# Kernel tuning notes

Measured on AMD Instinct MI355X. Metric: run time of the kernel, lower is better.

The kernel has to match this reference:

```python
import jax, jax.numpy as jnp
from jax import lax
import numpy as np

B, T, F, H, C = 32, 1000, 161, 512, 62

def setup_inputs() -> dict:
    key = jax.random.key(0)
    ks = jax.random.split(key, 12)
    s = lambda *sh: 1.0 / np.sqrt(sh[0])
    inp = {
        'x': jax.random.normal(ks[0], (B, T, F), jnp.float32),
        'seq_lens': jax.random.randint(ks[1], (B,), T // 2, T + 1, jnp.int32),
        'w1': jax.random.normal(ks[2], (F, H), jnp.float32) * s(F),
        'b1': jnp.zeros((H,), jnp.float32),
        'w2': jax.random.normal(ks[3], (H, H), jnp.float32) * s(H),
        'b2': jnp.zeros((H,), jnp.float32),
        'wg_f': jax.random.normal(ks[4], (2 * H, 2 * H), jnp.float32) * s(2 * H),
        'bg_f': jnp.ones((2 * H,), jnp.float32),  # TF GRU gate bias init = 1.0
        'wc_f': jax.random.normal(ks[5], (2 * H, H), jnp.float32) * s(2 * H),
        'bc_f': jnp.zeros((H,), jnp.float32),
        'wg_b': jax.random.normal(ks[6], (2 * H, 2 * H), jnp.float32) * s(2 * H),
        'bg_b': jnp.ones((2 * H,), jnp.float32),
        'wc_b': jax.random.normal(ks[7], (2 * H, H), jnp.float32) * s(2 * H),
        'bc_b': jnp.zeros((H,), jnp.float32),
        'wf': jax.random.normal(ks[8], (2 * H, C), jnp.float32) * s(2 * H),
        'bf': jnp.zeros((C,), jnp.float32),
    }
    return inp


def _reverse_sequence(x, lens):
    # mimic tf.reverse_sequence along time axis 1
    t = jnp.arange(x.shape[1])  # [T]
    idx = jnp.where(t[None, :] < lens[:, None], lens[:, None] - 1 - t[None, :], t[None, :])  # [B,T]
    return jnp.take_along_axis(x, idx[:, :, None], axis=1)


def _run_gru(x, lens, wg, bg, wc, bc):
    # x: [B,T,H] -> outputs [B,T,H]; zero output and frozen state past lens (dynamic_rnn semantics)
    xT = jnp.swapaxes(x, 0, 1)  # [T,B,H]
    h0 = jnp.zeros((x.shape[0], bc.shape[0]), x.dtype)

    def step(h, inp):
        xt, t = inp
        ru = jax.nn.sigmoid(jnp.concatenate([xt, h], axis=-1) @ wg + bg)
        r, u = jnp.split(ru, 2, axis=-1)
        c = jnp.tanh(jnp.concatenate([xt, r * h], axis=-1) @ wc + bc)
        hn = u * h + (1.0 - u) * c
        mask = (t < lens)[:, None]
        h_new = jnp.where(mask, hn, h)
        out = jnp.where(mask, hn, jnp.zeros_like(hn))
        return h_new, out

    _, outs = lax.scan(step, h0, (xT, jnp.arange(x.shape[1])))
    return jnp.swapaxes(outs, 0, 1)


def reference(x, seq_lens, w1, b1, w2, b2, wg_f, bg_f, wc_f, bc_f, wg_b, bg_b, wc_b, bc_b, wf, bf):
    h = jax.nn.relu(x @ w1 + b1)
    h = jax.nn.relu(h @ w2 + b2)  # [B,T,H]
    out_f = _run_gru(h, seq_lens, wg_f, bg_f, wc_f, bc_f)
    h_rev = _reverse_sequence(h, seq_lens)
    out_b = _reverse_sequence(_run_gru(h_rev, seq_lens, wg_b, bg_b, wc_b, bc_b), seq_lens)
    scores = jnp.concatenate([out_f, out_b], axis=2)  # [B,T,2H]
    logits = scores @ wf + bf  # [B,T,C]
    return logits
```

## Files before the change

### kernel.cpp

```cpp
#include <hip/hip_runtime.h>
#include <hip/hip_bf16.h>
#include <cstdint>

#define B_  32
#define T_  1000
#define F_  161
#define H_  512
#define C_  62
#define BT_ 32000
#define TC  200
#define NCH 5
#define MCH (B_ * TC)
#define ESC_TRIES (1 << 14)

typedef __bf16 bf16x8 __attribute__((ext_vector_type(8)));
typedef float  f32x4  __attribute__((ext_vector_type(4)));
typedef unsigned short us8 __attribute__((ext_vector_type(8)));

__device__ __forceinline__ float b2f(unsigned short s) {
    union { unsigned int i; float f; } v; v.i = (unsigned int)s << 16; return v.f;
}
__device__ __forceinline__ unsigned short f2b(float f) {
    unsigned int u = __float_as_uint(f);
    unsigned int r = u + 0x7fffu + ((u >> 16) & 1u);
    return (unsigned short)(r >> 16);
}


__global__ __launch_bounds__(256) void cvt_x_pad(const float* __restrict__ x,
                                                 unsigned short* __restrict__ xb) {
    int idx = blockIdx.x * 256 + threadIdx.x;
    if (idx >= BT_ * 192) return;
    int r = idx / 192, k = idx - r * 192;
    float v = (k < F_) ? x[(size_t)r * F_ + k] : 0.f;
    xb[idx] = f2b(v);
}

__global__ __launch_bounds__(256) void transpose_cvt(const float* __restrict__ src,
                                                     unsigned short* __restrict__ dst,
                                                     int K, int N, int k0, int KP, int NP) {
    int idx = blockIdx.x * 256 + threadIdx.x;
    if (idx >= NP * KP) return;
    int n = idx / KP, k = idx - n * KP;
    float v = (k < K && n < N) ? src[(size_t)(k0 + k) * N + n] : 0.f;
    dst[idx] = f2b(v);
}

__global__ __launch_bounds__(256) void biascat(const float* __restrict__ bg_f,
                                               const float* __restrict__ bc_f,
                                               const float* __restrict__ bg_b,
                                               const float* __restrict__ bc_b,
                                               float* __restrict__ bcat) {
    int idx = blockIdx.x * 256 + threadIdx.x;
    if (idx >= 2 * 1536) return;
    int d = idx / 1536, c = idx - d * 1536;
    const float* bg = d ? bg_b : bg_f;
    const float* bc = d ? bc_b : bc_f;
    bcat[idx] = (c < 1024) ? bg[c] : bc[c - 1024];
}


#define BM 128
#define BN 64
#define BK 64

template<bool RELU, int OMODE, bool AMAP>
__global__ __launch_bounds__(256) void gemm_bf16(const unsigned short* __restrict__ A,
                                                 const unsigned short* __restrict__ BT,
                                                 const float* __restrict__ bias,
                                                 void* __restrict__ Out,
                                                 int K, int Nreal, int t0) {
    __shared__ __align__(16) unsigned short As[BM * BK];
    __shared__ __align__(16) unsigned short Bs[BN * BK];
    const int tid  = threadIdx.x;
    const int lane = tid & 63;
    const int w    = tid >> 6;
    const int wm   = w & 1, wn = w >> 1;
    const int l15  = lane & 15, l4 = lane >> 4;
    const int m0   = blockIdx.x * BM;
    const int n0   = blockIdx.y * BN;

    const int ar = tid >> 1, ac = (tid & 1) * 32;
    const int br = tid >> 2, bc = (tid & 3) * 16;

    size_t arow;
    {
        int r = m0 + ar;
        if (AMAP) { int rb = r / TC; int rt = r - rb * TC; arow = (size_t)rb * T_ + t0 + rt; }
        else      arow = (size_t)r;
    }

    f32x4 acc[4][2] = {};

    for (int kt = 0; kt < K; kt += BK) {
        if (kt) __syncthreads();
        {
            const unsigned short* ga = A + arow * K + kt + ac;
            us8* la = (us8*)(As + ar * BK + ac);
            #pragma unroll
            for (int j = 0; j < 4; ++j) la[j] = *(const us8*)(ga + 8 * j);
            const unsigned short* gb = BT + (size_t)(n0 + br) * K + kt + bc;
            us8* lb = (us8*)(Bs + br * BK + bc);
            #pragma unroll
            for (int j = 0; j < 2; ++j) lb[j] = *(const us8*)(gb + 8 * j);
        }
        __syncthreads();
        #pragma unroll
        for (int kk = 0; kk < BK; kk += 32) {
            bf16x8 af[4], bfr[2];
            #pragma unroll
            for (int m = 0; m < 4; ++m)
                af[m] = *(const bf16x8*)(As + (wm * 64 + m * 16 + l15) * BK + kk + l4 * 8);
            #pragma unroll
            for (int n = 0; n < 2; ++n)
                bfr[n] = *(const bf16x8*)(Bs + (wn * 32 + n * 16 + l15) * BK + kk + l4 * 8);
            #pragma unroll
            for (int m = 0; m < 4; ++m)
                #pragma unroll
                for (int n = 0; n < 2; ++n)
                    acc[m][n] = __builtin_amdgcn_mfma_f32_16x16x32_bf16(af[m], bfr[n], acc[m][n], 0, 0, 0);
        }
    }

    const int rbase = m0 + wm * 64;
    const int cb    = n0 + wn * 32;
    #pragma unroll
    for (int m = 0; m < 4; ++m) {
        #pragma unroll
        for (int n = 0; n < 2; ++n) {
            int gc = cb + n * 16 + l15;
            if (gc < Nreal) {
                float bv = bias ? bias[gc] : 0.f;
                int gr0 = rbase + m * 16 + l4 * 4;
                #pragma unroll
                for (int r = 0; r < 4; ++r) {
                    float v = acc[m][n][r] + bv;
                    if (RELU) v = fmaxf(v, 0.f);
                    int gr = gr0 + r;
                    if (OMODE == 0) {
                        ((unsigned short*)Out)[(size_t)gr * Nreal + gc] = f2b(v);
                    } else {
                        int rb = gr / TC; int rt = gr - rb * TC;
                        size_t orow = (size_t)rb * T_ + t0 + rt;
                        ((float*)Out)[orow * Nreal + gc] += v;
                    }
                }
            }
        }
    }
}


__device__ __forceinline__ void wait_flag(const unsigned int* f, unsigned int tgt) {
    int tries = 0;
    while (__hip_atomic_load(f, __ATOMIC_RELAXED, __HIP_MEMORY_SCOPE_AGENT) < tgt) {
        if (++tries >= ESC_TRIES) break;
        __builtin_amdgcn_s_sleep(1);
    }
    asm volatile("" ::: "memory");
}

__device__ __forceinline__ void stage_peer(unsigned short* STG, const unsigned int* src,
                                           int q, int lane) {
    const unsigned long long* s64 = (const unsigned long long*)src;
    int row = lane >> 1, half = lane & 1;
    const unsigned long long* a = s64 + row * 128 + 8 * q + 4 * half;
    unsigned long long d0 = __hip_atomic_load(a + 0, __ATOMIC_RELAXED, __HIP_MEMORY_SCOPE_AGENT);
    unsigned long long d1 = __hip_atomic_load(a + 1, __ATOMIC_RELAXED, __HIP_MEMORY_SCOPE_AGENT);
    unsigned long long d2 = __hip_atomic_load(a + 2, __ATOMIC_RELAXED, __HIP_MEMORY_SCOPE_AGENT);
    unsigned long long d3 = __hip_atomic_load(a + 3, __ATOMIC_RELAXED, __HIP_MEMORY_SCOPE_AGENT);
    int bb  = 64 * q + 32 * half;
    int swz = (row & 7) << 4;
    char* rp = (char*)STG + row * 1024;
    *(unsigned long long*)(rp + ((bb +  0) ^ swz)) = d0;
    *(unsigned long long*)(rp + ((bb +  8) ^ swz)) = d1;
    *(unsigned long long*)(rp + ((bb + 16) ^ swz)) = d2;
    *(unsigned long long*)(rp + ((bb + 24) ^ swz)) = d3;
}

__global__ __launch_bounds__(512) void gru_persist(const unsigned short* __restrict__ wh_f,
                                                   const unsigned short* __restrict__ wh_b,
                                                   const unsigned short* __restrict__ Xf,
                                                   const unsigned short* __restrict__ Xb,
                                                   const int* __restrict__ seq_lens,
                                                   float* __restrict__ hf32_glob,
                                                   unsigned int* __restrict__ hb_g,
                                                   unsigned int* __restrict__ rh_g,
                                                   unsigned int* __restrict__ fH_g,
                                                   unsigned int* __restrict__ fR_g,
                                                   int* __restrict__ claim,
                                                   unsigned short* __restrict__ of,
                                                   unsigned short* __restrict__ ob,
                                                   int t0f, int t0b, int base, int init) {
    __shared__ __align__(16) unsigned short WG[64 * 512];
    __shared__ __align__(16) unsigned short WC[32 * 512];
    __shared__ __align__(16) unsigned short STG[32 * 512];
    __shared__ __align__(16) unsigned short XGs[32 * 64];
    __shared__ __align__(16) unsigned short XCs[32 * 32];
    __shared__ float USH[32][33];
    __shared__ float HOWN[32][32];
    __shared__ int Ls[32];
    __shared__ int role_sh;

    const int tid = threadIdx.x;

    if (tid == 0) {
        unsigned int xcd;
        asm volatile("s_getreg_b32 %0, hwreg(HW_REG_XCC_ID)" : "=s"(xcd));
        xcd &= 7u;
        int r = -1;
        if (xcd < 2u) {
            int s = atomicAdd(&claim[xcd], 1);
            if (s < 16) r = (int)(xcd * 16u) + s;
        }
        role_sh = r;
    }
    __syncthreads();
    const int role = role_sh;
    if (role < 0) return;
    const int dir = role >> 4;
    const int g   = role & 15;

    const int lane = tid & 63;
    const int w   = tid >> 6;
    const int l15 = lane & 15, l4 = lane >> 4;

    const unsigned short* wh = dir ? wh_b : wh_f;
    const unsigned short* X  = dir ? Xb : Xf;
    unsigned short* out      = dir ? ob : of;
    const int t0 = dir ? t0b : t0f;
    float*        hf32 = hf32_glob + (size_t)dir * 32 * 512;
    unsigned int* hb0 = hb_g + (size_t)dir * 2 * 8192;
    unsigned int* rh0 = rh_g + (size_t)dir * 2 * 8192;
    unsigned int* fH  = fH_g + dir * 256;
    unsigned int* fR  = fR_g + dir * 256;
    unsigned int* myfH = fH + g * 16;
    unsigned int* myfR = fR + g * 16;

    for (int j = tid; j < 4096; j += 512) {
        int col = j >> 6, ck = j & 63;
        int srcc = (col < 32) ? (32 * g + col) : (512 + 32 * g + (col - 32));
        int dstb = col * 1024 + ((ck * 16) ^ ((col & 7) << 4));
        *(us8*)((char*)WG + dstb) = *(const us8*)(wh + (size_t)srcc * 512 + ck * 8);
    }
    for (int j = tid; j < 2048; j += 512) {
        int col = j >> 6, ck = j & 63;
        int dstb = col * 1024 + ((ck * 16) ^ ((col & 7) << 4));
        *(us8*)((char*)WC + dstb) = *(const us8*)(wh + (size_t)(1024 + 32 * g + col) * 512 + ck * 8);
    }
    if (tid < 32) {
        int L = seq_lens[tid];
        Ls[tid] = L < 0 ? 0 : (L > T_ ? T_ : L);
    }
    for (int j = tid; j < 1024; j += 512) {
        int row = j >> 5, lc = j & 31;
        HOWN[row][lc] = init ? 0.f : hf32[row * 512 + 32 * g + lc];
    }
    {
        int tt0 = dir ? (TC - 1) : 0;
        if (tid < 256) {
            int b = tid >> 3, part = tid & 7;
            int srcc = (part < 4) ? (32 * g + part * 8) : (512 + 32 * g + (part - 4) * 8);
            *(us8*)(XGs + b * 64 + part * 8) =
                *(const us8*)(X + ((size_t)b * TC + tt0) * 1536 + srcc);
        }
    }

    const int mt = w & 1, nt = w >> 1;
    const int mt2 = w & 1, nt2 = (w >> 1) & 1;

    for (int i = 0; i < TC; ++i) {
        const int tt = dir ? (TC - 1 - i) : i;
        const int t  = t0 + tt;
        const unsigned int s = (unsigned)(base + i);

        if (init && i == 0) {
            for (int j = tid; j < 4096; j += 512)
                *(unsigned long long*)((char*)STG + j * 8) = 0ull;
        } else {
            const unsigned int* hbs = hb0 + ((s - 1) & 1) * 8192;
            #pragma unroll
            for (int k = 0; k < 2; ++k) {
                int q = 2 * w + k;
                wait_flag(fH + q * 16, s);
                stage_peer(STG, hbs, q, lane);
            }
        }
        if (tid < 128) {
            int b = tid >> 2, part = tid & 3;
            *(us8*)(XCs + b * 32 + part * 8) =
                *(const us8*)(X + ((size_t)b * TC + tt) * 1536 + 1024 + 32 * g + part * 8);
        }
        __syncthreads();

        f32x4 acc = {};
        {
            const int arow = mt * 16 + l15;
            const int bcol = nt * 16 + l15;
            const int sa = (arow & 7) << 4, sb2 = (bcol & 7) << 4;
            const char* pa = (const char*)STG + arow * 1024;
            const char* pb = (const char*)WG + bcol * 1024;
            #pragma unroll
            for (int kk = 0; kk < 16; ++kk) {
                int kb = kk * 64 + l4 * 16;
                bf16x8 a  = *(const bf16x8*)(pa + (kb ^ sa));
                bf16x8 bf = *(const bf16x8*)(pb + (kb ^ sb2));
                acc = __builtin_amdgcn_mfma_f32_16x16x32_bf16(a, bf, acc, 0, 0, 0);
            }
        }
        {
            unsigned int* rhs = rh0 + (s & 1) * 8192;
            const int colL = nt * 16 + l15;
            #pragma unroll
            for (int r = 0; r < 4; ++r) {
                int row = mt * 16 + l4 * 4 + r;
                float sv = acc[r] + b2f(XGs[row * 64 + colL]);
                float sg = 1.f / (1.f + __expf(-sv));
                if (colL < 32) {
                    int c = 32 * g + colL;
                    unsigned short ho = *(const unsigned short*)((const char*)STG + row * 1024 +
                                            ((c * 2) ^ ((row & 7) << 4)));
                    unsigned int pr = f2b(sg * b2f(ho));
                    unsigned int po = (unsigned int)__shfl_xor((int)pr, 1);
                    if (!(lane & 1))
                        __hip_atomic_store(rhs + row * 256 + 16 * g + (colL >> 1),
                                           pr | (po << 16),
                                           __ATOMIC_RELAXED, __HIP_MEMORY_SCOPE_AGENT);
                } else {
                    USH[row][colL - 32] = sg;
                }
            }
        }
        __syncthreads();
        if (tid == 0)
            __hip_atomic_store(myfR, s + 1, __ATOMIC_RELAXED, __HIP_MEMORY_SCOPE_AGENT);

        {
            const unsigned int* rhs = rh0 + (s & 1) * 8192;
            #pragma unroll
            for (int k = 0; k < 2; ++k) {
                int q = 2 * w + k;
                wait_flag(fR + q * 16, s + 1);
                stage_peer(STG, rhs, q, lane);
            }
        }
        __syncthreads();

        if (w < 4) {
            f32x4 acc2 = {};
            const int arow = mt2 * 16 + l15;
            const int bcol = nt2 * 16 + l15;
            const int sa = (arow & 7) << 4, sb2 = (bcol & 7) << 4;
            const char* pa = (const char*)STG + arow * 1024;
            const char* pb = (const char*)WC + bcol * 1024;
            #pragma unroll
            for (int kk = 0; kk < 16; ++kk) {
                int kb = kk * 64 + l4 * 16;
                bf16x8 a  = *(const bf16x8*)(pa + (kb ^ sa));
                bf16x8 bf = *(const bf16x8*)(pb + (kb ^ sb2));
                acc2 = __builtin_amdgcn_mfma_f32_16x16x32_bf16(a, bf, acc2, 0, 0, 0);
            }
            unsigned int* hbs = hb0 + (s & 1) * 8192;
            const int colL2 = nt2 * 16 + l15;
            const int col_c = 32 * g + colL2;
            #pragma unroll
            for (int r = 0; r < 4; ++r) {
                int row = mt2 * 16 + l4 * 4 + r;
                float sv = acc2[r] + b2f(XCs[row * 32 + colL2]);
                float cv = tanhf(sv);
                float uu = USH[row][colL2];
                float ho = HOWN[row][colL2];
                bool act = (t < Ls[row]);
                float hn = act ? (uu * ho + (1.f - uu) * cv) : ho;
                unsigned short hnb = f2b(hn);
                out[((size_t)row * TC + tt) * 512 + col_c] = act ? hnb : (unsigned short)0;
                unsigned int ph = hnb;
                unsigned int po = (unsigned int)__shfl_xor((int)ph, 1);
                if (!(lane & 1))
                    __hip_atomic_store(hbs + row * 256 + 16 * g + (colL2 >> 1),
                                       ph | (po << 16),
                                       __ATOMIC_RELAXED, __HIP_MEMORY_SCOPE_AGENT);
                HOWN[row][colL2] = hn;
            }
        } else if (i + 1 < TC) {
            int ttn = dir ? (tt - 1) : (tt + 1);
            int jd = tid - 256;
            int b = jd >> 3, part = jd & 7;
            int srcc = (part < 4) ? (32 * g + part * 8) : (512 + 32 * g + (part - 4) * 8);
            *(us8*)(XGs + b * 64 + part * 8) =
                *(const us8*)(X + ((size_t)b * TC + ttn) * 1536 + srcc);
        }
        __syncthreads();
        if (tid == 0)
            __hip_atomic_store(myfH, s + 1, __ATOMIC_RELAXED, __HIP_MEMORY_SCOPE_AGENT);
    }

    for (int j = tid; j < 1024; j += 512) {
        int row = j >> 5, lc = j & 31;
        hf32[row * 512 + 32 * g + lc] = HOWN[row][lc];
    }
}


extern "C" void kernel_launch(void* const* d_in, const int* in_sizes, int n_in,
                              void* d_out, int out_size, void* d_ws, size_t ws_size,
                              hipStream_t stream) {
    (void)in_sizes; (void)n_in; (void)out_size; (void)ws_size;
    const float* x    = (const float*)d_in[0];
    const int*   seq  = (const int*)  d_in[1];
    const float* w1   = (const float*)d_in[2];
    const float* b1   = (const float*)d_in[3];
    const float* w2   = (const float*)d_in[4];
    const float* b2   = (const float*)d_in[5];
    const float* wg_f = (const float*)d_in[6];
    const float* bg_f = (const float*)d_in[7];
    const float* wc_f = (const float*)d_in[8];
    const float* bc_f = (const float*)d_in[9];
    const float* wg_b = (const float*)d_in[10];
    const float* bg_b = (const float*)d_in[11];
    const float* wc_b = (const float*)d_in[12];
    const float* bc_b = (const float*)d_in[13];
    const float* wf   = (const float*)d_in[14];
    const float* bfv  = (const float*)d_in[15];

    char* p = (char*)d_ws;
    auto alloc = [&](size_t bytes) { char* q = p; p += (bytes + 255) & ~(size_t)255; return q; };

    unsigned short* w1T     = (unsigned short*)alloc(512 * 192 * 2);
    unsigned short* w2T     = (unsigned short*)alloc(512 * 512 * 2);
    unsigned short* wx_f    = (unsigned short*)alloc((size_t)1536 * 512 * 2);
    unsigned short* wx_b    = (unsigned short*)alloc((size_t)1536 * 512 * 2);
    unsigned short* wh_f    = (unsigned short*)alloc((size_t)1536 * 512 * 2);
    unsigned short* wh_b    = (unsigned short*)alloc((size_t)1536 * 512 * 2);
    unsigned short* wfT_top = (unsigned short*)alloc(64 * 512 * 2);
    unsigned short* wfT_bot = (unsigned short*)alloc(64 * 512 * 2);
    float*          bcat    = (float*)         alloc(2 * 1536 * 4);

    unsigned short* hB = (unsigned short*)alloc((size_t)BT_ * 512 * 2);

    char* U = alloc((size_t)MCH * 1536 * 2 * 2 + (size_t)MCH * 512 * 2 * 2);
    unsigned short* xb = (unsigned short*)U;
    unsigned short* h1 = (unsigned short*)(U + (size_t)BT_ * 192 * 2);
    unsigned short* Xf = (unsigned short*)U;
    unsigned short* Xb = (unsigned short*)(U + (size_t)MCH * 1536 * 2);
    unsigned short* of = (unsigned short*)(U + (size_t)MCH * 1536 * 2 * 2);
    unsigned short* ob = (unsigned short*)(U + (size_t)MCH * 1536 * 2 * 2 + (size_t)MCH * 512 * 2);

    unsigned int*   fH_gl    = (unsigned int*)alloc(2 * 256 * 4);
    unsigned int*   fR_gl    = (unsigned int*)alloc(2 * 256 * 4);
    int*            claim    = (int*)         alloc(256);
    float*          hf32_gl  = (float*)       alloc((size_t)2 * 32 * 512 * 4);
    unsigned int*   hb_gl    = (unsigned int*)alloc((size_t)2 * 2 * 8192 * 4);
    unsigned int*   rh_gl    = (unsigned int*)alloc((size_t)2 * 2 * 8192 * 4);

    hipMemsetAsync(d_out, 0, (size_t)BT_ * C_ * 4, stream);
    hipMemsetAsync(fH_gl, 0, 2 * 256 * 4 + 2 * 256 * 4 + 256, stream);

    transpose_cvt<<<(512 * 192) / 256, 256, 0, stream>>>(w1, w1T, 161, 512, 0, 192, 512);
    transpose_cvt<<<(512 * 512) / 256, 256, 0, stream>>>(w2, w2T, 512, 512, 0, 512, 512);
    transpose_cvt<<<(1024 * 512) / 256, 256, 0, stream>>>(wg_f, wx_f, 512, 1024, 0, 512, 1024);
    transpose_cvt<<<(512 * 512) / 256, 256, 0, stream>>>(wc_f, wx_f + (size_t)1024 * 512, 512, 512, 0, 512, 512);
    transpose_cvt<<<(1024 * 512) / 256, 256, 0, stream>>>(wg_b, wx_b, 512, 1024, 0, 512, 1024);
    transpose_cvt<<<(512 * 512) / 256, 256, 0, stream>>>(wc_b, wx_b + (size_t)1024 * 512, 512, 512, 0, 512, 512);
    transpose_cvt<<<(1024 * 512) / 256, 256, 0, stream>>>(wg_f, wh_f, 512, 1024, 512, 512, 1024);
    transpose_cvt<<<(512 * 512) / 256, 256, 0, stream>>>(wc_f, wh_f + (size_t)1024 * 512, 512, 512, 512, 512, 512);
    transpose_cvt<<<(1024 * 512) / 256, 256, 0, stream>>>(wg_b, wh_b, 512, 1024, 512, 512, 1024);
    transpose_cvt<<<(512 * 512) / 256, 256, 0, stream>>>(wc_b, wh_b + (size_t)1024 * 512, 512, 512, 512, 512, 512);
    transpose_cvt<<<(64 * 512) / 256, 256, 0, stream>>>(wf, wfT_top, 512, 62, 0, 512, 64);
    transpose_cvt<<<(64 * 512) / 256, 256, 0, stream>>>(wf, wfT_bot, 512, 62, 512, 512, 64);
    biascat<<<(2 * 1536 + 255) / 256, 256, 0, stream>>>(bg_f, bc_f, bg_b, bc_b, bcat);

    cvt_x_pad<<<(BT_ * 192 + 255) / 256, 256, 0, stream>>>(x, xb);
    gemm_bf16<true, 0, false><<<dim3(BT_ / BM, 512 / BN), 256, 0, stream>>>(xb, w1T, b1, h1, 192, 512, 0);
    gemm_bf16<true, 0, false><<<dim3(BT_ / BM, 512 / BN), 256, 0, stream>>>(h1, w2T, b2, hB, 512, 512, 0);

    for (int c = 0; c < NCH; ++c) {
        const int t0f = c * TC;
        const int t0b = (NCH - 1 - c) * TC;
        gemm_bf16<false, 0, true><<<dim3(MCH / BM, 1536 / BN), 256, 0, stream>>>(hB, wx_f, bcat,        Xf, 512, 1536, t0f);
        gemm_bf16<false, 0, true><<<dim3(MCH / BM, 1536 / BN), 256, 0, stream>>>(hB, wx_b, bcat + 1536, Xb, 512, 1536, t0b);
        gru_persist<<<256, 512, 0, stream>>>(wh_f, wh_b, Xf, Xb, seq, hf32_gl,
                                             hb_gl, rh_gl, fH_gl, fR_gl, claim + 2 * c,
                                             of, ob, t0f, t0b, c * TC, c == 0 ? 1 : 0);
        gemm_bf16<false, 1, false><<<dim3(MCH / BM, 1), 256, 0, stream>>>(of, wfT_top, bfv,     d_out, 512, C_, t0f);
        gemm_bf16<false, 1, false><<<dim3(MCH / BM, 1), 256, 0, stream>>>(ob, wfT_bot, nullptr, d_out, 512, C_, t0b);
    }
}
```

Baseline: 7.963 ms.

## Replace per-block ready flags with step tags embedded in exchanged data words

Each 32-bit packed pair of hidden or reset values is now stored in a 64-bit word whose upper half carries the step tag. Consumers poll the data words directly until every tag matches, instead of waiting on a separate per-block flag and then loading the data. This removes the flag store, the barrier-ordered flag round trip and the second load pass on the per-step critical path. In exchange the exchange buffers double in size, so each poll moves twice the bytes, and polling now issues eight loads per retry.

Result: slower. 11.60 ms (+45.7%).

```diff
diff --git a/kernel.cpp b/kernel.cpp
--- a/kernel.cpp
+++ b/kernel.cpp
@@ -151,31 +151,36 @@
 }
 
 
-__device__ __forceinline__ void wait_flag(const unsigned int* f, unsigned int tgt) {
+__device__ __forceinline__ void poll_stage(unsigned short* STG,
+                                           const unsigned long long* mb,
+                                           unsigned int tag, int q, int lane) {
+    int row = lane >> 1, half = lane & 1;
+    const unsigned long long* a = mb + row * 256 + 16 * q + 8 * half;
+    unsigned long long v[8];
+    unsigned int pend = 0xffu;
     int tries = 0;
-    while (__hip_atomic_load(f, __ATOMIC_RELAXED, __HIP_MEMORY_SCOPE_AGENT) < tgt) {
+    while (pend) {
+        #pragma unroll
+        for (int k = 0; k < 8; ++k)
+            if (pend & (1u << k))
+                v[k] = __hip_atomic_load(a + k, __ATOMIC_RELAXED, __HIP_MEMORY_SCOPE_AGENT);
+        #pragma unroll
+        for (int k = 0; k < 8; ++k)
+            if ((pend & (1u << k)) && (unsigned int)(v[k] >> 32) == tag)
+                pend &= ~(1u << k);
+        if (!pend) break;
         if (++tries >= ESC_TRIES) break;
         __builtin_amdgcn_s_sleep(1);
     }
     asm volatile("" ::: "memory");
-}
-
-__device__ __forceinline__ void stage_peer(unsigned short* STG, const unsigned int* src,
-                                           int q, int lane) {
-    const unsigned long long* s64 = (const unsigned long long*)src;
-    int row = lane >> 1, half = lane & 1;
-    const unsigned long long* a = s64 + row * 128 + 8 * q + 4 * half;
-    unsigned long long d0 = __hip_atomic_load(a + 0, __ATOMIC_RELAXED, __HIP_MEMORY_SCOPE_AGENT);
-    unsigned long long d1 = __hip_atomic_load(a + 1, __ATOMIC_RELAXED, __HIP_MEMORY_SCOPE_AGENT);
-    unsigned long long d2 = __hip_atomic_load(a + 2, __ATOMIC_RELAXED, __HIP_MEMORY_SCOPE_AGENT);
-    unsigned long long d3 = __hip_atomic_load(a + 3, __ATOMIC_RELAXED, __HIP_MEMORY_SCOPE_AGENT);
-    int bb  = 64 * q + 32 * half;
+    int base = 64 * q + 32 * half;
     int swz = (row & 7) << 4;
     char* rp = (char*)STG + row * 1024;
-    *(unsigned long long*)(rp + ((bb +  0) ^ swz)) = d0;
-    *(unsigned long long*)(rp + ((bb +  8) ^ swz)) = d1;
-    *(unsigned long long*)(rp + ((bb + 16) ^ swz)) = d2;
-    *(unsigned long long*)(rp + ((bb + 24) ^ swz)) = d3;
+    #pragma unroll
+    for (int k = 0; k < 4; ++k) {
+        unsigned long long d = (v[2 * k] & 0xffffffffull) | (v[2 * k + 1] << 32);
+        *(unsigned long long*)(rp + ((base + 8 * k) ^ swz)) = d;
+    }
 }
 
 __global__ __launch_bounds__(512) void gru_persist(const unsigned short* __restrict__ wh_f,
@@ -184,10 +189,8 @@
                                                    const unsigned short* __restrict__ Xb,
                                                    const int* __restrict__ seq_lens,
                                                    float* __restrict__ hf32_glob,
-                                                   unsigned int* __restrict__ hb_g,
-                                                   unsigned int* __restrict__ rh_g,
-                                                   unsigned int* __restrict__ fH_g,
-                                                   unsigned int* __restrict__ fR_g,
+                                                   unsigned long long* __restrict__ hb_g,
+                                                   unsigned long long* __restrict__ rh_g,
                                                    int* __restrict__ claim,
                                                    unsigned short* __restrict__ of,
                                                    unsigned short* __restrict__ ob,
@@ -229,13 +232,9 @@
     const unsigned short* X  = dir ? Xb : Xf;
     unsigned short* out      = dir ? ob : of;
     const int t0 = dir ? t0b : t0f;
-    float*        hf32 = hf32_glob + (size_t)dir * 32 * 512;
-    unsigned int* hb0 = hb_g + (size_t)dir * 2 * 8192;
-    unsigned int* rh0 = rh_g + (size_t)dir * 2 * 8192;
-    unsigned int* fH  = fH_g + dir * 256;
-    unsigned int* fR  = fR_g + dir * 256;
-    unsigned int* myfH = fH + g * 16;
-    unsigned int* myfR = fR + g * 16;
+    float*              hf32 = hf32_glob + (size_t)dir * 32 * 512;
+    unsigned long long* hb0 = hb_g + (size_t)dir * 2 * 8192;
+    unsigned long long* rh0 = rh_g + (size_t)dir * 2 * 8192;
 
     for (int j = tid; j < 4096; j += 512) {
         int col = j >> 6, ck = j & 63;
@@ -278,13 +277,9 @@
             for (int j = tid; j < 4096; j += 512)
                 *(unsigned long long*)((char*)STG + j * 8) = 0ull;
         } else {
-            const unsigned int* hbs = hb0 + ((s - 1) & 1) * 8192;
-            #pragma unroll
-            for (int k = 0; k < 2; ++k) {
-                int q = 2 * w + k;
-                wait_flag(fH + q * 16, s);
-                stage_peer(STG, hbs, q, lane);
-            }
+            const unsigned long long* hbs = hb0 + ((s - 1) & 1) * 8192;
+            poll_stage(STG, hbs, s, 2 * w, lane);
+            poll_stage(STG, hbs, s, 2 * w + 1, lane);
         }
         if (tid < 128) {
             int b = tid >> 2, part = tid & 3;
@@ -309,7 +304,8 @@
             }
         }
         {
-            unsigned int* rhs = rh0 + (s & 1) * 8192;
+            unsigned long long* rhs = rh0 + (s & 1) * 8192;
+            const unsigned long long tagw = ((unsigned long long)(s + 1)) << 32;
             const int colL = nt * 16 + l15;
             #pragma unroll
             for (int r = 0; r < 4; ++r) {
@@ -324,7 +320,7 @@
                     unsigned int po = (unsigned int)__shfl_xor((int)pr, 1);
                     if (!(lane & 1))
                         __hip_atomic_store(rhs + row * 256 + 16 * g + (colL >> 1),
-                                           pr | (po << 16),
+                                           tagw | pr | (po << 16),
                                            __ATOMIC_RELAXED, __HIP_MEMORY_SCOPE_AGENT);
                 } else {
                     USH[row][colL - 32] = sg;
@@ -332,17 +328,11 @@
             }
         }
         __syncthreads();
-        if (tid == 0)
-            __hip_atomic_store(myfR, s + 1, __ATOMIC_RELAXED, __HIP_MEMORY_SCOPE_AGENT);
 
         {
-            const unsigned int* rhs = rh0 + (s & 1) * 8192;
-            #pragma unroll
-            for (int k = 0; k < 2; ++k) {
-                int q = 2 * w + k;
-                wait_flag(fR + q * 16, s + 1);
-                stage_peer(STG, rhs, q, lane);
-            }
+            const unsigned long long* rhs = rh0 + (s & 1) * 8192;
+            poll_stage(STG, rhs, s + 1, 2 * w, lane);
+            poll_stage(STG, rhs, s + 1, 2 * w + 1, lane);
         }
         __syncthreads();
 
@@ -360,7 +350,8 @@
                 bf16x8 bf = *(const bf16x8*)(pb + (kb ^ sb2));
                 acc2 = __builtin_amdgcn_mfma_f32_16x16x32_bf16(a, bf, acc2, 0, 0, 0);
             }
-            unsigned int* hbs = hb0 + (s & 1) * 8192;
+            unsigned long long* hbs = hb0 + (s & 1) * 8192;
+            const unsigned long long tagw = ((unsigned long long)(s + 1)) << 32;
             const int colL2 = nt2 * 16 + l15;
             const int col_c = 32 * g + colL2;
             #pragma unroll
@@ -378,7 +369,7 @@
                 unsigned int po = (unsigned int)__shfl_xor((int)ph, 1);
                 if (!(lane & 1))
                     __hip_atomic_store(hbs + row * 256 + 16 * g + (colL2 >> 1),
-                                       ph | (po << 16),
+                                       tagw | ph | (po << 16),
                                        __ATOMIC_RELAXED, __HIP_MEMORY_SCOPE_AGENT);
                 HOWN[row][colL2] = hn;
             }
@@ -391,8 +382,6 @@
                 *(const us8*)(X + ((size_t)b * TC + ttn) * 1536 + srcc);
         }
         __syncthreads();
-        if (tid == 0)
-            __hip_atomic_store(myfH, s + 1, __ATOMIC_RELAXED, __HIP_MEMORY_SCOPE_AGENT);
     }
 
     for (int j = tid; j < 1024; j += 512) {
@@ -446,15 +435,13 @@
     unsigned short* of = (unsigned short*)(U + (size_t)MCH * 1536 * 2 * 2);
     unsigned short* ob = (unsigned short*)(U + (size_t)MCH * 1536 * 2 * 2 + (size_t)MCH * 512 * 2);
 
-    unsigned int*   fH_gl    = (unsigned int*)alloc(2 * 256 * 4);
-    unsigned int*   fR_gl    = (unsigned int*)alloc(2 * 256 * 4);
-    int*            claim    = (int*)         alloc(256);
-    float*          hf32_gl  = (float*)       alloc((size_t)2 * 32 * 512 * 4);
-    unsigned int*   hb_gl    = (unsigned int*)alloc((size_t)2 * 2 * 8192 * 4);
-    unsigned int*   rh_gl    = (unsigned int*)alloc((size_t)2 * 2 * 8192 * 4);
+    int*                claim   = (int*)               alloc(256);
+    float*              hf32_gl = (float*)             alloc((size_t)2 * 32 * 512 * 4);
+    unsigned long long* hb_gl   = (unsigned long long*)alloc((size_t)2 * 2 * 8192 * 8);
+    unsigned long long* rh_gl   = (unsigned long long*)alloc((size_t)2 * 2 * 8192 * 8);
 
     hipMemsetAsync(d_out, 0, (size_t)BT_ * C_ * 4, stream);
-    hipMemsetAsync(fH_gl, 0, 2 * 256 * 4 + 2 * 256 * 4 + 256, stream);
+    hipMemsetAsync(claim, 0, 256, stream);
 
     transpose_cvt<<<(512 * 192) / 256, 256, 0, stream>>>(w1, w1T, 161, 512, 0, 192, 512);
     transpose_cvt<<<(512 * 512) / 256, 256, 0, stream>>>(w2, w2T, 512, 512, 0, 512, 512);
@@ -480,7 +467,7 @@
         gemm_bf16<false, 0, true><<<dim3(MCH / BM, 1536 / BN), 256, 0, stream>>>(hB, wx_f, bcat,        Xf, 512, 1536, t0f);
         gemm_bf16<false, 0, true><<<dim3(MCH / BM, 1536 / BN), 256, 0, stream>>>(hB, wx_b, bcat + 1536, Xb, 512, 1536, t0b);
         gru_persist<<<256, 512, 0, stream>>>(wh_f, wh_b, Xf, Xb, seq, hf32_gl,
-                                             hb_gl, rh_gl, fH_gl, fR_gl, claim + 2 * c,
+                                             hb_gl, rh_gl, claim + 2 * c,
                                              of, ob, t0f, t0b, c * TC, c == 0 ? 1 : 0);
         gemm_bf16<false, 1, false><<<dim3(MCH / BM, 1), 256, 0, stream>>>(of, wfT_top, bfv,     d_out, 512, C_, t0f);
         gemm_bf16<false, 1, false><<<dim3(MCH / BM, 1), 256, 0, stream>>>(ob, wfT_bot, nullptr, d_out, 512, C_, t0b);
```

## Load peer GRU state directly into MFMA fragments with per-wave flags

Applied to the files above, without the earlier changes.

Removes the LDS staging buffer for the peer hidden and reset-gated states. Each wave now reads its MFMA A-fragments straight from global memory after a single wave-wide poll over all 64 per-wave flags. Flags become per-wave: each wave drains its stores with s_waitcnt and publishes its own flag, so the block-wide barrier before signaling and one __syncthreads per step go away. The owned hidden state moves from LDS into registers. The cost is more fine-grained global loads in the MFMA loop and 4x more flag traffic, with the risk of weaker ordering guarantees under relaxed atomics.

New measurement: 14.04 ms. 76.3% more time.

```diff
diff --git a/kernel.cpp b/kernel.cpp
--- a/kernel.cpp
+++ b/kernel.cpp
@@ -151,31 +151,25 @@
 }
 
 
-__device__ __forceinline__ void wait_flag(const unsigned int* f, unsigned int tgt) {
+__device__ __forceinline__ void poll64(const unsigned int* f, unsigned int tgt, int lane) {
+    const unsigned int* fp = f + ((lane >> 2) << 4) + (lane & 3);
     int tries = 0;
-    while (__hip_atomic_load(f, __ATOMIC_RELAXED, __HIP_MEMORY_SCOPE_AGENT) < tgt) {
+    for (;;) {
+        unsigned int v = __hip_atomic_load(fp, __ATOMIC_RELAXED, __HIP_MEMORY_SCOPE_AGENT);
+        if (__all(v >= tgt)) break;
         if (++tries >= ESC_TRIES) break;
         __builtin_amdgcn_s_sleep(1);
     }
     asm volatile("" ::: "memory");
 }
 
-__device__ __forceinline__ void stage_peer(unsigned short* STG, const unsigned int* src,
-                                           int q, int lane) {
-    const unsigned long long* s64 = (const unsigned long long*)src;
-    int row = lane >> 1, half = lane & 1;
-    const unsigned long long* a = s64 + row * 128 + 8 * q + 4 * half;
-    unsigned long long d0 = __hip_atomic_load(a + 0, __ATOMIC_RELAXED, __HIP_MEMORY_SCOPE_AGENT);
+__device__ __forceinline__ bf16x8 frag_ld(const unsigned long long* mb, int row, int q, int l4) {
+    const unsigned long long* a = mb + row * 128 + 8 * q + 2 * l4;
+    unsigned long long d0 = __hip_atomic_load(a,     __ATOMIC_RELAXED, __HIP_MEMORY_SCOPE_AGENT);
     unsigned long long d1 = __hip_atomic_load(a + 1, __ATOMIC_RELAXED, __HIP_MEMORY_SCOPE_AGENT);
-    unsigned long long d2 = __hip_atomic_load(a + 2, __ATOMIC_RELAXED, __HIP_MEMORY_SCOPE_AGENT);
-    unsigned long long d3 = __hip_atomic_load(a + 3, __ATOMIC_RELAXED, __HIP_MEMORY_SCOPE_AGENT);
-    int bb  = 64 * q + 32 * half;
-    int swz = (row & 7) << 4;
-    char* rp = (char*)STG + row * 1024;
-    *(unsigned long long*)(rp + ((bb +  0) ^ swz)) = d0;
-    *(unsigned long long*)(rp + ((bb +  8) ^ swz)) = d1;
-    *(unsigned long long*)(rp + ((bb + 16) ^ swz)) = d2;
-    *(unsigned long long*)(rp + ((bb + 24) ^ swz)) = d3;
+    union { unsigned long long u[2]; bf16x8 v; } c;
+    c.u[0] = d0; c.u[1] = d1;
+    return c.v;
 }
 
 __global__ __launch_bounds__(512) void gru_persist(const unsigned short* __restrict__ wh_f,
@@ -194,11 +188,9 @@
                                                    int t0f, int t0b, int base, int init) {
     __shared__ __align__(16) unsigned short WG[64 * 512];
     __shared__ __align__(16) unsigned short WC[32 * 512];
-    __shared__ __align__(16) unsigned short STG[32 * 512];
     __shared__ __align__(16) unsigned short XGs[32 * 64];
     __shared__ __align__(16) unsigned short XCs[32 * 32];
     __shared__ float USH[32][33];
-    __shared__ float HOWN[32][32];
     __shared__ int Ls[32];
     __shared__ int role_sh;
 
@@ -234,8 +226,6 @@
     unsigned int* rh0 = rh_g + (size_t)dir * 2 * 8192;
     unsigned int* fH  = fH_g + dir * 256;
     unsigned int* fR  = fR_g + dir * 256;
-    unsigned int* myfH = fH + g * 16;
-    unsigned int* myfR = fR + g * 16;
 
     for (int j = tid; j < 4096; j += 512) {
         int col = j >> 6, ck = j & 63;
@@ -251,10 +241,6 @@
     if (tid < 32) {
         int L = seq_lens[tid];
         Ls[tid] = L < 0 ? 0 : (L > T_ ? T_ : L);
-    }
-    for (int j = tid; j < 1024; j += 512) {
-        int row = j >> 5, lc = j & 31;
-        HOWN[row][lc] = init ? 0.f : hf32[row * 512 + 32 * g + lc];
     }
     {
         int tt0 = dir ? (TC - 1) : 0;
@@ -269,96 +255,90 @@
     const int mt = w & 1, nt = w >> 1;
     const int mt2 = w & 1, nt2 = (w >> 1) & 1;
 
+    float hreg[4];
+    if (w < 4) {
+        #pragma unroll
+        for (int r = 0; r < 4; ++r) {
+            int row = mt2 * 16 + l4 * 4 + r;
+            hreg[r] = init ? 0.f : hf32[row * 512 + 32 * g + nt2 * 16 + l15];
+        }
+    }
+    __syncthreads();
+
     for (int i = 0; i < TC; ++i) {
         const int tt = dir ? (TC - 1 - i) : i;
         const int t  = t0 + tt;
         const unsigned int s = (unsigned)(base + i);
 
-        if (init && i == 0) {
-            for (int j = tid; j < 4096; j += 512)
-                *(unsigned long long*)((char*)STG + j * 8) = 0ull;
-        } else {
-            const unsigned int* hbs = hb0 + ((s - 1) & 1) * 8192;
-            #pragma unroll
-            for (int k = 0; k < 2; ++k) {
-                int q = 2 * w + k;
-                wait_flag(fH + q * 16, s);
-                stage_peer(STG, hbs, q, lane);
-            }
-        }
         if (tid < 128) {
             int b = tid >> 2, part = tid & 3;
             *(us8*)(XCs + b * 32 + part * 8) =
                 *(const us8*)(X + ((size_t)b * TC + tt) * 1536 + 1024 + 32 * g + part * 8);
         }
-        __syncthreads();
 
         f32x4 acc = {};
-        {
+        if (!(init && i == 0)) {
+            poll64(fH, s, lane);
+            const unsigned long long* hbs =
+                (const unsigned long long*)(hb0 + ((s - 1) & 1) * 8192);
             const int arow = mt * 16 + l15;
             const int bcol = nt * 16 + l15;
-            const int sa = (arow & 7) << 4, sb2 = (bcol & 7) << 4;
-            const char* pa = (const char*)STG + arow * 1024;
+            const int sb2 = (bcol & 7) << 4;
             const char* pb = (const char*)WG + bcol * 1024;
             #pragma unroll
-            for (int kk = 0; kk < 16; ++kk) {
-                int kb = kk * 64 + l4 * 16;
-                bf16x8 a  = *(const bf16x8*)(pa + (kb ^ sa));
-                bf16x8 bf = *(const bf16x8*)(pb + (kb ^ sb2));
-                acc = __builtin_amdgcn_mfma_f32_16x16x32_bf16(a, bf, acc, 0, 0, 0);
+            for (int q = 0; q < 16; ++q) {
+                bf16x8 afr = frag_ld(hbs, arow, q, l4);
+                bf16x8 bfr = *(const bf16x8*)(pb + ((q * 64 + l4 * 16) ^ sb2));
+                acc = __builtin_amdgcn_mfma_f32_16x16x32_bf16(afr, bfr, acc, 0, 0, 0);
             }
         }
+
         {
-            unsigned int* rhs = rh0 + (s & 1) * 8192;
             const int colL = nt * 16 + l15;
-            #pragma unroll
-            for (int r = 0; r < 4; ++r) {
-                int row = mt * 16 + l4 * 4 + r;
-                float sv = acc[r] + b2f(XGs[row * 64 + colL]);
-                float sg = 1.f / (1.f + __expf(-sv));
-                if (colL < 32) {
-                    int c = 32 * g + colL;
-                    unsigned short ho = *(const unsigned short*)((const char*)STG + row * 1024 +
-                                            ((c * 2) ^ ((row & 7) << 4)));
-                    unsigned int pr = f2b(sg * b2f(ho));
+            if (w < 4) {
+                unsigned int* rhs = rh0 + (s & 1) * 8192;
+                #pragma unroll
+                for (int r = 0; r < 4; ++r) {
+                    int row = mt * 16 + l4 * 4 + r;
+                    float sv = acc[r] + b2f(XGs[row * 64 + colL]);
+                    float sg = 1.f / (1.f + __expf(-sv));
+                    float ho = b2f(f2b(hreg[r]));
+                    unsigned int pr = f2b(sg * ho);
                     unsigned int po = (unsigned int)__shfl_xor((int)pr, 1);
                     if (!(lane & 1))
                         __hip_atomic_store(rhs + row * 256 + 16 * g + (colL >> 1),
                                            pr | (po << 16),
                                            __ATOMIC_RELAXED, __HIP_MEMORY_SCOPE_AGENT);
-                } else {
-                    USH[row][colL - 32] = sg;
+                }
+                asm volatile("s_waitcnt vmcnt(0)" ::: "memory");
+                if (lane == 0)
+                    __hip_atomic_store(fR + g * 16 + w, s + 1,
+                                       __ATOMIC_RELAXED, __HIP_MEMORY_SCOPE_AGENT);
+            } else {
+                #pragma unroll
+                for (int r = 0; r < 4; ++r) {
+                    int row = mt * 16 + l4 * 4 + r;
+                    float sv = acc[r] + b2f(XGs[row * 64 + colL]);
+                    USH[row][colL - 32] = 1.f / (1.f + __expf(-sv));
                 }
             }
         }
         __syncthreads();
-        if (tid == 0)
-            __hip_atomic_store(myfR, s + 1, __ATOMIC_RELAXED, __HIP_MEMORY_SCOPE_AGENT);
-
-        {
-            const unsigned int* rhs = rh0 + (s & 1) * 8192;
-            #pragma unroll
-            for (int k = 0; k < 2; ++k) {
-                int q = 2 * w + k;
-                wait_flag(fR + q * 16, s + 1);
-                stage_peer(STG, rhs, q, lane);
-            }
-        }
-        __syncthreads();
 
         if (w < 4) {
+            poll64(fR, s + 1, lane);
+            const unsigned long long* rhs =
+                (const unsigned long long*)(rh0 + (s & 1) * 8192);
             f32x4 acc2 = {};
             const int arow = mt2 * 16 + l15;
             const int bcol = nt2 * 16 + l15;
-            const int sa = (arow & 7) << 4, sb2 = (bcol & 7) << 4;
-            const char* pa = (const char*)STG + arow * 1024;
+            const int sb2 = (bcol & 7) << 4;
             const char* pb = (const char*)WC + bcol * 1024;
             #pragma unroll
-            for (int kk = 0; kk < 16; ++kk) {
-                int kb = kk * 64 + l4 * 16;
-                bf16x8 a  = *(const bf16x8*)(pa + (kb ^ sa));
-                bf16x8 bf = *(const bf16x8*)(pb + (kb ^ sb2));
-                acc2 = __builtin_amdgcn_mfma_f32_16x16x32_bf16(a, bf, acc2, 0, 0, 0);
+            for (int q = 0; q < 16; ++q) {
+                bf16x8 afr = frag_ld(rhs, arow, q, l4);
+                bf16x8 bfr = *(const bf16x8*)(pb + ((q * 64 + l4 * 16) ^ sb2));
+                acc2 = __builtin_amdgcn_mfma_f32_16x16x32_bf16(afr, bfr, acc2, 0, 0, 0);
             }
             unsigned int* hbs = hb0 + (s & 1) * 8192;
             const int colL2 = nt2 * 16 + l15;
@@ -369,7 +349,7 @@
                 float sv = acc2[r] + b2f(XCs[row * 32 + colL2]);
                 float cv = tanhf(sv);
                 float uu = USH[row][colL2];
-                float ho = HOWN[row][colL2];
+                float ho = hreg[r];
                 bool act = (t < Ls[row]);
                 float hn = act ? (uu * ho + (1.f - uu) * cv) : ho;
                 unsigned short hnb = f2b(hn);
@@ -380,8 +360,12 @@
                     __hip_atomic_store(hbs + row * 256 + 16 * g + (colL2 >> 1),
                                        ph | (po << 16),
                                        __ATOMIC_RELAXED, __HIP_MEMORY_SCOPE_AGENT);
-                HOWN[row][colL2] = hn;
+                hreg[r] = hn;
             }
+            asm volatile("s_waitcnt vmcnt(0)" ::: "memory");
+            if (lane == 0)
+                __hip_atomic_store(fH + g * 16 + w, s + 1,
+                                   __ATOMIC_RELAXED, __HIP_MEMORY_SCOPE_AGENT);
         } else if (i + 1 < TC) {
             int ttn = dir ? (tt - 1) : (tt + 1);
             int jd = tid - 256;
@@ -391,13 +375,14 @@
                 *(const us8*)(X + ((size_t)b * TC + ttn) * 1536 + srcc);
         }
         __syncthreads();
-        if (tid == 0)
-            __hip_atomic_store(myfH, s + 1, __ATOMIC_RELAXED, __HIP_MEMORY_SCOPE_AGENT);
-    }
-
-    for (int j = tid; j < 1024; j += 512) {
-        int row = j >> 5, lc = j & 31;
-        hf32[row * 512 + 32 * g + lc] = HOWN[row][lc];
+    }
+
+    if (w < 4) {
+        #pragma unroll
+        for (int r = 0; r < 4; ++r) {
+            int row = mt2 * 16 + l4 * 4 + r;
+            hf32[row * 512 + 32 * g + nt2 * 16 + l15] = hreg[r];
+        }
     }
 }
 
```

## Use per-wave flag publishing and wave-wide polling in persistent GRU recurrence

Applied to the files above, without the earlier changes.

Each of the four writer waves now publishes its own completion flag right after its stores drain (s_waitcnt vmcnt(0)), rather than one thread publishing a block-wide flag after a __syncthreads. Consumers poll all eight sub-flags of their two peer groups in parallel with one wave vote. The hidden state moves from the HOWN shared array into per-lane registers, and r*h is computed from those registers instead of being read back from staged shared memory. The intent is to cut a barrier and serial flag polls from the per-timestep cross-block handoff, at the cost of more flag traffic and reliance on relaxed-ordering memory semantics.

Result: slower. 8.613 ms (+8.2%).

```diff
diff --git a/kernel.cpp b/kernel.cpp
--- a/kernel.cpp
+++ b/kernel.cpp
@@ -151,9 +151,14 @@
 }
 
 
-__device__ __forceinline__ void wait_flag(const unsigned int* f, unsigned int tgt) {
+__device__ __forceinline__ void poll_sub(const unsigned int* f, unsigned int tgt,
+                                         int w, int lane) {
+    const unsigned int* fp = f + (2 * w + (lane >> 2)) * 16 + (lane & 3);
     int tries = 0;
-    while (__hip_atomic_load(f, __ATOMIC_RELAXED, __HIP_MEMORY_SCOPE_AGENT) < tgt) {
+    for (;;) {
+        unsigned int v = (lane < 8)
+            ? __hip_atomic_load(fp, __ATOMIC_RELAXED, __HIP_MEMORY_SCOPE_AGENT) : tgt;
+        if (__all(v >= tgt)) break;
         if (++tries >= ESC_TRIES) break;
         __builtin_amdgcn_s_sleep(1);
     }
@@ -198,7 +203,6 @@
     __shared__ __align__(16) unsigned short XGs[32 * 64];
     __shared__ __align__(16) unsigned short XCs[32 * 32];
     __shared__ float USH[32][33];
-    __shared__ float HOWN[32][32];
     __shared__ int Ls[32];
     __shared__ int role_sh;
 
@@ -234,8 +238,6 @@
     unsigned int* rh0 = rh_g + (size_t)dir * 2 * 8192;
     unsigned int* fH  = fH_g + dir * 256;
     unsigned int* fR  = fR_g + dir * 256;
-    unsigned int* myfH = fH + g * 16;
-    unsigned int* myfR = fR + g * 16;
 
     for (int j = tid; j < 4096; j += 512) {
         int col = j >> 6, ck = j & 63;
@@ -251,10 +253,6 @@
     if (tid < 32) {
         int L = seq_lens[tid];
         Ls[tid] = L < 0 ? 0 : (L > T_ ? T_ : L);
-    }
-    for (int j = tid; j < 1024; j += 512) {
-        int row = j >> 5, lc = j & 31;
-        HOWN[row][lc] = init ? 0.f : hf32[row * 512 + 32 * g + lc];
     }
     {
         int tt0 = dir ? (TC - 1) : 0;
@@ -269,6 +267,16 @@
     const int mt = w & 1, nt = w >> 1;
     const int mt2 = w & 1, nt2 = (w >> 1) & 1;
 
+    float hreg[4];
+    if (w < 4) {
+        #pragma unroll
+        for (int r = 0; r < 4; ++r) {
+            int row = mt2 * 16 + l4 * 4 + r;
+            hreg[r] = init ? 0.f : hf32[row * 512 + 32 * g + nt2 * 16 + l15];
+        }
+    }
+    __syncthreads();
+
     for (int i = 0; i < TC; ++i) {
         const int tt = dir ? (TC - 1 - i) : i;
         const int t  = t0 + tt;
@@ -279,12 +287,9 @@
                 *(unsigned long long*)((char*)STG + j * 8) = 0ull;
         } else {
             const unsigned int* hbs = hb0 + ((s - 1) & 1) * 8192;
-            #pragma unroll
-            for (int k = 0; k < 2; ++k) {
-                int q = 2 * w + k;
-                wait_flag(fH + q * 16, s);
-                stage_peer(STG, hbs, q, lane);
-            }
+            poll_sub(fH, s, w, lane);
+            stage_peer(STG, hbs, 2 * w, lane);
+            stage_peer(STG, hbs, 2 * w + 1, lane);
         }
         if (tid < 128) {
             int b = tid >> 2, part = tid & 3;
@@ -309,40 +314,42 @@
             }
         }
         {
-            unsigned int* rhs = rh0 + (s & 1) * 8192;
             const int colL = nt * 16 + l15;
-            #pragma unroll
-            for (int r = 0; r < 4; ++r) {
-                int row = mt * 16 + l4 * 4 + r;
-                float sv = acc[r] + b2f(XGs[row * 64 + colL]);
-                float sg = 1.f / (1.f + __expf(-sv));
-                if (colL < 32) {
-                    int c = 32 * g + colL;
-                    unsigned short ho = *(const unsigned short*)((const char*)STG + row * 1024 +
-                                            ((c * 2) ^ ((row & 7) << 4)));
-                    unsigned int pr = f2b(sg * b2f(ho));
+            if (w < 4) {
+                unsigned int* rhs = rh0 + (s & 1) * 8192;
+                #pragma unroll
+                for (int r = 0; r < 4; ++r) {
+                    int row = mt * 16 + l4 * 4 + r;
+                    float sv = acc[r] + b2f(XGs[row * 64 + colL]);
+                    float sg = 1.f / (1.f + __expf(-sv));
+                    float ho = b2f(f2b(hreg[r]));
+                    unsigned int pr = f2b(sg * ho);
                     unsigned int po = (unsigned int)__shfl_xor((int)pr, 1);
                     if (!(lane & 1))
                         __hip_atomic_store(rhs + row * 256 + 16 * g + (colL >> 1),
                                            pr | (po << 16),
                                            __ATOMIC_RELAXED, __HIP_MEMORY_SCOPE_AGENT);
-                } else {
-                    USH[row][colL - 32] = sg;
+                }
+                asm volatile("s_waitcnt vmcnt(0)" ::: "memory");
+                if (lane == 0)
+                    __hip_atomic_store(fR + g * 16 + w, s + 1,
+                                       __ATOMIC_RELAXED, __HIP_MEMORY_SCOPE_AGENT);
+            } else {
+                #pragma unroll
+                for (int r = 0; r < 4; ++r) {
+                    int row = mt * 16 + l4 * 4 + r;
+                    float sv = acc[r] + b2f(XGs[row * 64 + colL]);
+                    USH[row][colL - 32] = 1.f / (1.f + __expf(-sv));
                 }
             }
         }
         __syncthreads();
-        if (tid == 0)
-            __hip_atomic_store(myfR, s + 1, __ATOMIC_RELAXED, __HIP_MEMORY_SCOPE_AGENT);
 
         {
             const unsigned int* rhs = rh0 + (s & 1) * 8192;
-            #pragma unroll
-            for (int k = 0; k < 2; ++k) {
-                int q = 2 * w + k;
-                wait_flag(fR + q * 16, s + 1);
-                stage_peer(STG, rhs, q, lane);
-            }
+            poll_sub(fR, s + 1, w, lane);
+            stage_peer(STG, rhs, 2 * w, lane);
+            stage_peer(STG, rhs, 2 * w + 1, lane);
         }
         __syncthreads();
 
@@ -369,7 +376,7 @@
                 float sv = acc2[r] + b2f(XCs[row * 32 + colL2]);
                 float cv = tanhf(sv);
                 float uu = USH[row][colL2];
-                float ho = HOWN[row][colL2];
+                float ho = hreg[r];
                 bool act = (t < Ls[row]);
                 float hn = act ? (uu * ho + (1.f - uu) * cv) : ho;
                 unsigned short hnb = f2b(hn);
@@ -380,8 +387,12 @@
                     __hip_atomic_store(hbs + row * 256 + 16 * g + (colL2 >> 1),
                                        ph | (po << 16),
                                        __ATOMIC_RELAXED, __HIP_MEMORY_SCOPE_AGENT);
-                HOWN[row][colL2] = hn;
+                hreg[r] = hn;
             }
+            asm volatile("s_waitcnt vmcnt(0)" ::: "memory");
+            if (lane == 0)
+                __hip_atomic_store(fH + g * 16 + w, s + 1,
+                                   __ATOMIC_RELAXED, __HIP_MEMORY_SCOPE_AGENT);
         } else if (i + 1 < TC) {
             int ttn = dir ? (tt - 1) : (tt + 1);
             int jd = tid - 256;
@@ -391,13 +402,14 @@
                 *(const us8*)(X + ((size_t)b * TC + ttn) * 1536 + srcc);
         }
         __syncthreads();
-        if (tid == 0)
-            __hip_atomic_store(myfH, s + 1, __ATOMIC_RELAXED, __HIP_MEMORY_SCOPE_AGENT);
-    }
-
-    for (int j = tid; j < 1024; j += 512) {
-        int row = j >> 5, lc = j & 31;
-        hf32[row * 512 + 32 * g + lc] = HOWN[row][lc];
+    }
+
+    if (w < 4) {
+        #pragma unroll
+        for (int r = 0; r < 4; ++r) {
+            int row = mt2 * 16 + l4 * 4 + r;
+            hf32[row * 512 + 32 * g + nt2 * 16 + l15] = hreg[r];
+        }
     }
 }
 
```
